# Optimization experiments

Hardware: AMD Instinct MI355X
Metric: run time of the kernel (lower is better)

The kernel has to match this reference:

```python
import jax, jax.numpy as jnp
import numpy as np

B, S, D, H = 2, 2048, 1024, 16
DH = D // H  # dim per head (dim_singl_head)
SCALE = 0.02


def layer_norm(x, g, b, eps=1e-5):
    m = jnp.mean(x, axis=-1, keepdims=True)
    v = jnp.mean((x - m) ** 2, axis=-1, keepdims=True)
    return (x - m) / jnp.sqrt(v + eps) * g + b


def setup_inputs() -> dict:
    key = jax.random.key(0)
    ks = jax.random.split(key, 12)
    return {
        "query": jax.random.normal(ks[0], (B, S, D), jnp.float32),
        "key": jax.random.normal(ks[1], (B, S, D), jnp.float32),
        "value": jax.random.normal(ks[2], (B, S, D), jnp.float32),
        "mask": jax.random.randint(ks[3], (B, S), 0, 2).astype(jnp.int32),
        "Wq": jax.random.normal(ks[4], (D, D), jnp.float32) * SCALE,
        "bq": jnp.zeros((D,), jnp.float32),
        "Wk": jax.random.normal(ks[5], (D, D), jnp.float32) * SCALE,
        "bk": jnp.zeros((D,), jnp.float32),
        "Wv": jax.random.normal(ks[6], (D, D), jnp.float32) * SCALE,
        "bv": jnp.zeros((D,), jnp.float32),
        "g_att": jnp.ones((DH,), jnp.float32),
        "b_att": jnp.zeros((DH,), jnp.float32),
        "Wres": jax.random.normal(ks[7], (D, D), jnp.float32) * SCALE,
        "bres": jnp.zeros((D,), jnp.float32),
        "g_out": jnp.ones((D,), jnp.float32),
        "b_out": jnp.zeros((D,), jnp.float32),
    }


def reference(query, key, value, mask, Wq, bq, Wk, bk, Wv, bv,
              g_att, b_att, Wres, bres, g_out, b_out):
    # split heads: torch's split(dh,-1)+cat(dim=0) == [H,B,S,dh] layout
    def heads(x):
        return x.reshape(B, S, H, DH).transpose(2, 0, 1, 3)  # [H,B,S,dh]

    q = heads(query @ Wq + bq)
    k = heads(key @ Wk + bk)
    v = heads(value @ Wv + bv)

    # additive mask: (1-mask)*-1e9, broadcast [1,B,1,Sk]
    madd = (1.0 - mask.astype(q.dtype))[None, :, None, :] * -1e9

    scores = jnp.einsum('hbqd,hbkd->hbqk', q, k) / np.float32(np.sqrt(DH))
    w = jax.nn.softmax(scores + madd, axis=-1)
    out = jnp.einsum('hbqk,hbkd->hbqd', w, v)

    out = out + q                         # residual_att
    out = layer_norm(out, g_att, b_att)   # per-head LayerNorm on dh

    # concat heads back: [H,B,S,dh] -> [B,S,H*dh]
    out = out.transpose(1, 2, 0, 3).reshape(B, S, D)

    out = out + jnp.tanh(out @ Wres + bres)  # residual_out branch
    out = layer_norm(out, g_out, b_out)      # norm_out
    return jnp.tanh(out)                     # final activation
```

## Files before the change

### kernel.cpp

```cpp
#include <hip/hip_runtime.h>
#include <cstdint>
#include <cstddef>

#define BB 2
#define SS 2048
#define DD 1024
#define HH 16
#define DHH 64
#define MROWS (BB*SS)

typedef short short8 __attribute__((ext_vector_type(8)));
typedef short short4v __attribute__((ext_vector_type(4)));
typedef float floatx4 __attribute__((ext_vector_type(4)));
typedef float floatx16 __attribute__((ext_vector_type(16)));
typedef unsigned int uint4v __attribute__((ext_vector_type(4)));

#define GAS __attribute__((address_space(1)))
#define LAS __attribute__((address_space(3)))

__device__ __forceinline__ float4 ld4(const float* p) { return *(const float4*)p; }

__device__ __forceinline__ short f2bf(float x) {
    unsigned u = __builtin_bit_cast(unsigned, x);
    unsigned r = (u + 0x7fffu + ((u >> 16) & 1u)) >> 16;
    return (short)r;
}

__device__ __forceinline__ unsigned cvtpk(float lo, float hi) {
    unsigned r;
    asm("v_cvt_pk_bf16_f32 %0, %1, %2" : "=v"(r) : "v"(lo), "v"(hi));
    return r;
}

__device__ __forceinline__ void gl_lds16(const short* g, short* l) {
    __builtin_amdgcn_global_load_lds((const GAS unsigned int*)g,
                                     (LAS unsigned int*)l, 16, 0, 0);
}

__global__ __launch_bounds__(256) void convert_kernel(
    const float* __restrict__ s0, const float* __restrict__ s1, const float* __restrict__ s2,
    short* __restrict__ d0, short* __restrict__ d1, short* __restrict__ d2)
{
    const float* s; short* d;
    if (blockIdx.z == 0)      { s = s0; d = d0; }
    else if (blockIdx.z == 1) { s = s1; d = d1; }
    else                      { s = s2; d = d2; }
    size_t idx = ((size_t)blockIdx.x * 256 + threadIdx.x) * 8;
    float4 a = ld4(s + idx);
    float4 b = ld4(s + idx + 4);
    short8 p;
    p[0] = f2bf(a.x); p[1] = f2bf(a.y); p[2] = f2bf(a.z); p[3] = f2bf(a.w);
    p[4] = f2bf(b.x); p[5] = f2bf(b.y); p[6] = f2bf(b.z); p[7] = f2bf(b.w);
    *(short8*)(d + idx) = p;
}

__global__ __launch_bounds__(256) void transpose_w_kernel(
    const float* __restrict__ W0, const float* __restrict__ W1,
    const float* __restrict__ W2, const float* __restrict__ W3,
    short* __restrict__ T0, short* __restrict__ T1,
    short* __restrict__ T2, short* __restrict__ T3)
{
    const float* W; short* T;
    if (blockIdx.z == 0)      { W = W0; T = T0; }
    else if (blockIdx.z == 1) { W = W1; T = T1; }
    else if (blockIdx.z == 2) { W = W2; T = T2; }
    else                      { W = W3; T = T3; }

    __shared__ short tile[64 * 72];
    const int t  = threadIdx.x;
    const int k0 = blockIdx.x * 64, n0 = blockIdx.y * 64;
#pragma unroll
    for (int i = 0; i < 4; i++) {
        int flat = i * 256 + t;
        int row = flat >> 4;
        int c4  = (flat & 15) * 4;
        float4 v = ld4(W + (size_t)(k0 + row) * DD + n0 + c4);
        tile[(c4 + 0) * 72 + row] = f2bf(v.x);
        tile[(c4 + 1) * 72 + row] = f2bf(v.y);
        tile[(c4 + 2) * 72 + row] = f2bf(v.z);
        tile[(c4 + 3) * 72 + row] = f2bf(v.w);
    }
    __syncthreads();
#pragma unroll
    for (int i = 0; i < 4; i++) {
        int flat = i * 256 + t;
        int nrow = flat >> 4;
        int kc   = (flat & 15) * 4;
        short4v pk = *(short4v*)&tile[nrow * 72 + kc];
        *(short4v*)(T + (size_t)(n0 + nrow) * DD + k0 + kc) = pk;
    }
}

__global__ __launch_bounds__(256) void gemm_bf16_kernel(
    const short* __restrict__ A0, const short* __restrict__ A1, const short* __restrict__ A2,
    const short* __restrict__ Bt0, const short* __restrict__ Bt1, const short* __restrict__ Bt2,
    const float* __restrict__ b0, const float* __restrict__ b1, const float* __restrict__ b2,
    float* __restrict__ Cf0, float* __restrict__ Cf1, float* __restrict__ Cf2,
    short* __restrict__ Cb0, short* __restrict__ Cb1, short* __restrict__ Cb2,
    short* __restrict__ Ct0, short* __restrict__ Ct1, short* __restrict__ Ct2,
    float cs0, float cs1, float cs2)
{
    const short* A; const short* Bt; const float* bias;
    float* Cf; short* Cb; short* Ct; float cbs;
    if (blockIdx.z == 0)      { A = A0; Bt = Bt0; bias = b0; Cf = Cf0; Cb = Cb0; Ct = Ct0; cbs = cs0; }
    else if (blockIdx.z == 1) { A = A1; Bt = Bt1; bias = b1; Cf = Cf1; Cb = Cb1; Ct = Ct1; cbs = cs1; }
    else                      { A = A2; Bt = Bt2; bias = b2; Cf = Cf2; Cb = Cb2; Ct = Ct2; cbs = cs2; }

    __shared__ __align__(16) short As[128 * 32];
    __shared__ __align__(16) short Bs[128 * 32];

    const int tid  = threadIdx.x;
    const int lane = tid & 63;
    const int wave = tid >> 6;
    const int quad = lane >> 4;
    const int l15  = lane & 15;
    const int m0 = blockIdx.y * 128;
    const int n0 = blockIdx.x * 128;
    const int wr = (wave >> 1) * 64;
    const int wc = (wave & 1) * 64;

    floatx4 acc[4][4];
#pragma unroll
    for (int mt = 0; mt < 4; mt++)
#pragma unroll
        for (int nt = 0; nt < 4; nt++) acc[mt][nt] = (floatx4)0.0f;

    for (int k0 = 0; k0 < DD; k0 += 32) {
        __syncthreads();
#pragma unroll
        for (int j = 0; j < 2; j++) {
            int chunk = j * 256 + tid;
            int row = chunk >> 2;
            int ch  = chunk & 3;
            gl_lds16(A  + (size_t)(m0 + row) * DD + k0 + ch * 8, &As[chunk * 8]);
            gl_lds16(Bt + (size_t)(n0 + row) * DD + k0 + ch * 8, &Bs[chunk * 8]);
        }
        __syncthreads();

        short8 af[4], bf[4];
#pragma unroll
        for (int mt = 0; mt < 4; mt++)
            af[mt] = *(const short8*)&As[(wr + mt * 16 + l15) * 32 + quad * 8];
#pragma unroll
        for (int nt = 0; nt < 4; nt++)
            bf[nt] = *(const short8*)&Bs[(wc + nt * 16 + l15) * 32 + quad * 8];
#pragma unroll
        for (int mt = 0; mt < 4; mt++)
#pragma unroll
            for (int nt = 0; nt < 4; nt++)
                acc[mt][nt] = __builtin_amdgcn_mfma_f32_16x16x32_bf16(af[mt], bf[nt], acc[mt][nt], 0, 0, 0);
    }

    float biasv[4];
#pragma unroll
    for (int nt = 0; nt < 4; nt++) biasv[nt] = bias[n0 + wc + nt * 16 + l15];

    if (Cf || Cb) {
#pragma unroll
        for (int mt = 0; mt < 4; mt++)
#pragma unroll
            for (int r = 0; r < 4; r++) {
                const int m = m0 + wr + mt * 16 + quad * 4 + r;
                const size_t rowb = (size_t)m * DD + n0 + wc;
#pragma unroll
                for (int nt = 0; nt < 4; nt++) {
                    float v = acc[mt][nt][r] + biasv[nt];
                    if (Cf) Cf[rowb + nt * 16 + l15] = v;
                    if (Cb) Cb[rowb + nt * 16 + l15] = f2bf(v * cbs);
                }
            }
    }
    if (Ct) {
#pragma unroll
        for (int mt = 0; mt < 4; mt++) {
            const int mbase = m0 + wr + mt * 16 + quad * 4;
            const int bb = mbase >> 11;
            const int s0 = mbase & 2047;
#pragma unroll
            for (int nt = 0; nt < 4; nt++) {
                const int c = n0 + wc + nt * 16 + l15;
                short4v pk;
#pragma unroll
                for (int r = 0; r < 4; r++) pk[r] = f2bf(acc[mt][nt][r] + biasv[nt]);
                *(short4v*)(Ct + ((size_t)(bb * 1024 + c)) * SS + s0) = pk;
            }
        }
    }
}

__global__ __launch_bounds__(256, 2) void attn_mfma_kernel(
    const short* __restrict__ Qb, const short* __restrict__ Kb, const short* __restrict__ Vt,
    const float* __restrict__ Qf, const int* __restrict__ mask,
    const float* __restrict__ g_att, const float* __restrict__ b_att,
    float* __restrict__ X, short* __restrict__ Xb)
{
    const int tid  = threadIdx.x;
    const int lane = tid & 63;
    const int wave = tid >> 6;
    const int hi   = lane >> 5;
    const int c    = lane & 31;

    const int h  = blockIdx.y;
    const int b  = blockIdx.z;
    const int q0 = blockIdx.x * 128;
    const int bS = b * SS;

    __shared__ __align__(16) short Ks[2 * 64 * 72];
    __shared__ __align__(16) short Vs[2 * 64 * 72];
    __shared__ float smadd[2 * 64];

    short8 qf[4];
#pragma unroll
    for (int ks = 0; ks < 4; ks++)
        qf[ks] = *(const short8*)(Qb +
            (size_t)(bS + q0 + wave * 32 + c) * DD + h * 64 + ks * 16 + hi * 8);

    floatx16 o[2];
    o[0] = (floatx16)0.0f;
    o[1] = (floatx16)0.0f;
    float lsum = 0.0f;

    const int srow = tid >> 3;
    const int sch  = tid & 7;

    short8 kreg[2], vreg[2];
    float mreg;
    {
#pragma unroll
        for (int i = 0; i < 2; i++) {
            int row = srow + i * 32;
            kreg[i] = *(const short8*)(Kb + (size_t)(bS + row) * DD + h * 64 + sch * 8);
            vreg[i] = *(const short8*)(Vt + (size_t)(b * 1024 + h * 64 + row) * SS + sch * 8);
        }
        mreg = (tid < 64) ? (float)mask[bS + tid] : 0.0f;
    }

    for (int kt = 0; kt < SS / 64; kt++) {
        const int bufo = (kt & 1) * (64 * 72);
#pragma unroll
        for (int i = 0; i < 2; i++) {
            int row = srow + i * 32;
            *(short8*)&Ks[bufo + row * 72 + sch * 8] = kreg[i];
            *(short8*)&Vs[bufo + row * 72 + sch * 8] = vreg[i];
        }
        if (tid < 64) smadd[(kt & 1) * 64 + tid] = (1.0f - mreg) * -1e9f;

        if (kt < SS / 64 - 1) {
            const int k0n = (kt + 1) * 64;
#pragma unroll
            for (int i = 0; i < 2; i++) {
                int row = srow + i * 32;
                kreg[i] = *(const short8*)(Kb + (size_t)(bS + k0n + row) * DD + h * 64 + sch * 8);
                vreg[i] = *(const short8*)(Vt + (size_t)(b * 1024 + h * 64 + row) * SS + k0n + sch * 8);
            }
            mreg = (tid < 64) ? (float)mask[bS + k0n + tid] : 0.0f;
        }

        __builtin_amdgcn_s_waitcnt(0xC07F);
        __builtin_amdgcn_s_barrier();

#pragma unroll
        for (int g = 0; g < 2; g++) {
            floatx16 acc = (floatx16)0.0f;
#pragma unroll
            for (int ks = 0; ks < 4; ks++) {
                short8 kf = *(const short8*)&Ks[bufo + (g * 32 + c) * 72 + ks * 16 + hi * 8];
                acc = __builtin_amdgcn_mfma_f32_32x32x16_bf16(kf, qf[ks], acc, 0, 0, 0);
            }
            float p[16];
#pragma unroll
            for (int a = 0; a < 4; a++) {
                float4 mr = *(const float4*)&smadd[(kt & 1) * 64 + g * 32 + a * 8 + hi * 4];
                p[4 * a + 0] = __builtin_exp2f(acc[4 * a + 0] + mr.x);
                p[4 * a + 1] = __builtin_exp2f(acc[4 * a + 1] + mr.y);
                p[4 * a + 2] = __builtin_exp2f(acc[4 * a + 2] + mr.z);
                p[4 * a + 3] = __builtin_exp2f(acc[4 * a + 3] + mr.w);
            }
            lsum += ((p[0] + p[1]) + (p[2] + p[3])) + ((p[4] + p[5]) + (p[6] + p[7]))
                  + ((p[8] + p[9]) + (p[10] + p[11])) + ((p[12] + p[13]) + (p[14] + p[15]));

#pragma unroll
            for (int t = 0; t < 2; t++) {
                unsigned w0 = cvtpk(p[8 * t + 0], p[8 * t + 1]);
                unsigned w1 = cvtpk(p[8 * t + 2], p[8 * t + 3]);
                unsigned w2 = cvtpk(p[8 * t + 4], p[8 * t + 5]);
                unsigned w3 = cvtpk(p[8 * t + 6], p[8 * t + 7]);
                asm volatile("v_permlane32_swap_b32 %0, %1" : "+v"(w0), "+v"(w2));
                asm volatile("v_permlane32_swap_b32 %0, %1" : "+v"(w1), "+v"(w3));
                uint4v u = {w0, w1, w2, w3};
                short8 pa = __builtin_bit_cast(short8, u);
#pragma unroll
                for (int dg = 0; dg < 2; dg++) {
                    short8 vb = *(const short8*)&Vs[bufo + (dg * 32 + c) * 72
                                                    + (g * 2 + t) * 16 + hi * 8];
                    o[dg] = __builtin_amdgcn_mfma_f32_32x32x16_bf16(pa, vb, o[dg], 0, 0, 0);
                }
            }
        }
    }

    lsum += __shfl_xor(lsum, 32);
    const float rl = 1.0f / lsum;

    const float g0v = g_att[c], g1v = g_att[32 + c];
    const float b0v = b_att[c], b1v = b_att[32 + c];

#pragma unroll
    for (int r = 0; r < 16; r++) {
        const int rloc = (r & 3) + 8 * (r >> 2) + 4 * hi;
        const float rlr = __shfl(rl, rloc);
        const int row = q0 + wave * 32 + rloc;
        const size_t base = (size_t)(bS + row) * DD + h * 64;
        float x0 = o[0][r] * rlr + Qf[base + c];
        float x1 = o[1][r] * rlr + Qf[base + 32 + c];
        float s = x0 + x1;
#pragma unroll
        for (int off = 1; off < 32; off <<= 1) s += __shfl_xor(s, off);
        const float mu = s * (1.0f / 64.0f);
        float d0 = x0 - mu, d1 = x1 - mu;
        float v = d0 * d0 + d1 * d1;
#pragma unroll
        for (int off = 1; off < 32; off <<= 1) v += __shfl_xor(v, off);
        const float rstd = rsqrtf(v * (1.0f / 64.0f) + 1e-5f);
        float y0 = d0 * rstd * g0v + b0v;
        float y1 = d1 * rstd * g1v + b1v;
        X[base + c]      = y0;
        X[base + 32 + c] = y1;
        Xb[base + c]      = f2bf(y0);
        Xb[base + 32 + c] = f2bf(y1);
    }
}

__global__ __launch_bounds__(256) void lnout_kernel(
    const float* __restrict__ X, const float* __restrict__ Y,
    const float* __restrict__ g, const float* __restrict__ bcoef,
    float* __restrict__ out)
{
    const int r = blockIdx.x;
    const int t = threadIdx.x;
    const size_t base = (size_t)r * DD + (t << 2);
    float4 x = ld4(X + base);
    float4 y = ld4(Y + base);
    float4 z;
    z.x = x.x + tanhf(y.x);
    z.y = x.y + tanhf(y.y);
    z.z = x.z + tanhf(y.z);
    z.w = x.w + tanhf(y.w);

    __shared__ float red[4];
    __shared__ float stats[2];
    const int w = t >> 6;

    float sv = z.x + z.y + z.z + z.w;
#pragma unroll
    for (int off = 32; off > 0; off >>= 1) sv += __shfl_down(sv, off);
    if ((t & 63) == 0) red[w] = sv;
    __syncthreads();
    if (t == 0) stats[0] = (red[0] + red[1] + red[2] + red[3]) * (1.0f / 1024.0f);
    __syncthreads();
    const float mu = stats[0];

    float4 d;
    d.x = z.x - mu; d.y = z.y - mu; d.z = z.z - mu; d.w = z.w - mu;
    float s2 = d.x * d.x + d.y * d.y + d.z * d.z + d.w * d.w;
#pragma unroll
    for (int off = 32; off > 0; off >>= 1) s2 += __shfl_down(s2, off);
    if ((t & 63) == 0) red[w] = s2;
    __syncthreads();
    if (t == 0) stats[1] = rsqrtf((red[0] + red[1] + red[2] + red[3]) * (1.0f / 1024.0f) + 1e-5f);
    __syncthreads();
    const float rstd = stats[1];

    float4 gv = ld4(g + (t << 2));
    float4 bv = ld4(bcoef + (t << 2));
    float4 o;
    o.x = tanhf(d.x * rstd * gv.x + bv.x);
    o.y = tanhf(d.y * rstd * gv.y + bv.y);
    o.z = tanhf(d.z * rstd * gv.z + bv.z);
    o.w = tanhf(d.w * rstd * gv.w + bv.w);
    *(float4*)(out + base) = o;
}

extern "C" void kernel_launch(void* const* d_in, const int* in_sizes, int n_in,
                              void* d_out, int out_size, void* d_ws, size_t ws_size,
                              hipStream_t stream)
{
    const float* query = (const float*)d_in[0];
    const float* key   = (const float*)d_in[1];
    const float* value = (const float*)d_in[2];
    const int*   mask  = (const int*)  d_in[3];
    const float* Wq    = (const float*)d_in[4];
    const float* bq    = (const float*)d_in[5];
    const float* Wk    = (const float*)d_in[6];
    const float* bk    = (const float*)d_in[7];
    const float* Wv    = (const float*)d_in[8];
    const float* bv    = (const float*)d_in[9];
    const float* g_att = (const float*)d_in[10];
    const float* b_att = (const float*)d_in[11];
    const float* Wres  = (const float*)d_in[12];
    const float* bres  = (const float*)d_in[13];
    const float* g_out = (const float*)d_in[14];
    const float* b_out = (const float*)d_in[15];

    const size_t MAT = (size_t)MROWS * DD;
    float* fws = (float*)d_ws;
    float* Qw = fws;
    float* Xw = fws + MAT;
    short* Qb = (short*)(fws + 2 * MAT);
    short* Kb = Qb + MAT;
    short* Vt = Kb + MAT;
    short* qbf = Vt + MAT;
    short* kbf = qbf + MAT;
    short* vbf = kbf + MAT;
    short* Wtq = vbf + MAT;
    short* Wtk = Wtq + DD * DD;
    short* Wtv = Wtk + DD * DD;
    short* Wtr = Wtv + DD * DD;
    short* Xb = qbf;
    float* Yw = (float*)kbf;

    convert_kernel<<<dim3(MAT / 2048, 1, 3), 256, 0, stream>>>(
        query, key, value, qbf, kbf, vbf);

    transpose_w_kernel<<<dim3(16, 16, 4), 256, 0, stream>>>(
        Wq, Wk, Wv, Wres, Wtq, Wtk, Wtv, Wtr);

    gemm_bf16_kernel<<<dim3(8, 32, 3), 256, 0, stream>>>(
        qbf, kbf, vbf, Wtq, Wtk, Wtv, bq, bk, bv,
        Qw, nullptr, nullptr,
        Qb, Kb, nullptr,
        nullptr, nullptr, Vt,
        0.180336884f, 1.0f, 1.0f);

    attn_mfma_kernel<<<dim3(SS / 128, HH, BB), 256, 0, stream>>>(
        Qb, Kb, Vt, Qw, mask, g_att, b_att, Xw, Xb);

    gemm_bf16_kernel<<<dim3(8, 32, 1), 256, 0, stream>>>(
        Xb, Xb, Xb, Wtr, Wtr, Wtr, bres, bres, bres,
        Yw, Yw, Yw, nullptr, nullptr, nullptr, nullptr, nullptr, nullptr,
        1.0f, 1.0f, 1.0f);

    lnout_kernel<<<MROWS, 256, 0, stream>>>(Xw, Yw, g_out, b_out, (float*)d_out);
}
```

Before: 290.3 us.

## Repack K/V into MFMA fragment layout and stream directly from global into registers

Adds a repack kernel that rearranges K and transposed V into per-head, per-tile MFMA fragment order and precomputes the additive mask as floats. The attention kernel then drops its LDS staging, double buffering and barriers, loading fragments with coalesced per-lane global reads into registers, software-pipelined one tile ahead, with MFMA sections raised via s_setprio. This trades LDS traffic and block synchronisation for an extra kernel launch, more register pressure, and redundant global/L2 reads since each block now fetches its own K/V fragments.

```diff
diff --git a/kernel.cpp b/kernel.cpp
--- a/kernel.cpp
+++ b/kernel.cpp
@@ -188,9 +188,91 @@
     }
 }
 
+__global__ __launch_bounds__(256) void repack_kernel(
+    const short* __restrict__ Kb, const short* __restrict__ Vt,
+    const int* __restrict__ mask,
+    short* __restrict__ Kf, short* __restrict__ Vf, float* __restrict__ maddf)
+{
+    const int t = threadIdx.x;
+    if (blockIdx.z == 0) {
+        const int b = blockIdx.x >> 6, kg = blockIdx.x & 63;
+#pragma unroll
+        for (int i = 0; i < 16; i++) {
+            const int h = i, ks = t >> 6, lane = t & 63;
+            const int c = lane & 31, hi = lane >> 5;
+            short8 v = *(const short8*)(Kb + (size_t)(b * 2048 + kg * 32 + c) * 1024
+                                        + h * 64 + ks * 16 + hi * 8);
+            *(short8*)(Kf + ((size_t)((b * 16 + h) * 64 + kg)) * 2048 + ks * 512 + lane * 8) = v;
+        }
+    } else if (blockIdx.x < 64) {
+        const int b = blockIdx.x >> 5, kt = blockIdx.x & 31;
+#pragma unroll
+        for (int i = 0; i < 32; i++) {
+            const int flat = i * 256 + t;
+            const int h = flat >> 9, rest = flat & 511;
+            const int tp = rest >> 7, dg = (rest >> 6) & 1, lane = rest & 63;
+            const int c = lane & 31, hi = lane >> 5;
+            short8 v = *(const short8*)(Vt + (size_t)(b * 1024 + h * 64 + dg * 32 + c) * 2048
+                                        + kt * 64 + tp * 16 + hi * 8);
+            *(short8*)(Vf + ((size_t)((b * 16 + h) * 32 + kt)) * 4096
+                       + (tp * 2 + dg) * 512 + lane * 8) = v;
+        }
+    } else if (blockIdx.x < 66) {
+        const int b = blockIdx.x - 64;
+#pragma unroll
+        for (int j = 0; j < 8; j++) {
+            const int idx = t * 8 + j;
+            maddf[b * 2048 + idx] = (1.0f - (float)mask[b * 2048 + idx]) * -1e9f;
+        }
+    }
+}
+
+__device__ __forceinline__ void attn_tile(
+    const short8 (&kf)[2][4], const short8 (&vf)[8], const short8 (&qf)[4],
+    const float* mdb, int kt, floatx16 (&o)[2], float& lsum)
+{
+#pragma unroll
+    for (int g = 0; g < 2; g++) {
+        floatx16 acc = (floatx16)0.0f;
+        __builtin_amdgcn_s_setprio(1);
+#pragma unroll
+        for (int ks = 0; ks < 4; ks++)
+            acc = __builtin_amdgcn_mfma_f32_32x32x16_bf16(kf[g][ks], qf[ks], acc, 0, 0, 0);
+        __builtin_amdgcn_s_setprio(0);
+        float p[16];
+#pragma unroll
+        for (int a = 0; a < 4; a++) {
+            float4 mr = *(const float4*)(mdb + kt * 64 + g * 32 + a * 8);
+            p[4 * a + 0] = __builtin_exp2f(acc[4 * a + 0] + mr.x);
+            p[4 * a + 1] = __builtin_exp2f(acc[4 * a + 1] + mr.y);
+            p[4 * a + 2] = __builtin_exp2f(acc[4 * a + 2] + mr.z);
+            p[4 * a + 3] = __builtin_exp2f(acc[4 * a + 3] + mr.w);
+        }
+        lsum += ((p[0] + p[1]) + (p[2] + p[3])) + ((p[4] + p[5]) + (p[6] + p[7]))
+              + ((p[8] + p[9]) + (p[10] + p[11])) + ((p[12] + p[13]) + (p[14] + p[15]));
+#pragma unroll
+        for (int t2 = 0; t2 < 2; t2++) {
+            unsigned w0 = cvtpk(p[8 * t2 + 0], p[8 * t2 + 1]);
+            unsigned w1 = cvtpk(p[8 * t2 + 2], p[8 * t2 + 3]);
+            unsigned w2 = cvtpk(p[8 * t2 + 4], p[8 * t2 + 5]);
+            unsigned w3 = cvtpk(p[8 * t2 + 6], p[8 * t2 + 7]);
+            asm volatile("v_permlane32_swap_b32 %0, %1" : "+v"(w0), "+v"(w2));
+            asm volatile("v_permlane32_swap_b32 %0, %1" : "+v"(w1), "+v"(w3));
+            uint4v u = {w0, w1, w2, w3};
+            short8 pa = __builtin_bit_cast(short8, u);
+            __builtin_amdgcn_s_setprio(1);
+#pragma unroll
+            for (int dg = 0; dg < 2; dg++)
+                o[dg] = __builtin_amdgcn_mfma_f32_32x32x16_bf16(
+                    pa, vf[(g * 2 + t2) * 2 + dg], o[dg], 0, 0, 0);
+            __builtin_amdgcn_s_setprio(0);
+        }
+    }
+}
+
 __global__ __launch_bounds__(256, 2) void attn_mfma_kernel(
-    const short* __restrict__ Qb, const short* __restrict__ Kb, const short* __restrict__ Vt,
-    const float* __restrict__ Qf, const int* __restrict__ mask,
+    const short* __restrict__ Qb, const short* __restrict__ Kf, const short* __restrict__ Vf,
+    const float* __restrict__ Qf, const float* __restrict__ maddf,
     const float* __restrict__ g_att, const float* __restrict__ b_att,
     float* __restrict__ X, short* __restrict__ Xb)
 {
@@ -205,9 +287,9 @@
     const int q0 = blockIdx.x * 128;
     const int bS = b * SS;
 
-    __shared__ __align__(16) short Ks[2 * 64 * 72];
-    __shared__ __align__(16) short Vs[2 * 64 * 72];
-    __shared__ float smadd[2 * 64];
+    const short* kfb = Kf + ((size_t)(b * 16 + h) * 64) * 2048 + lane * 8;
+    const short* vfb = Vf + ((size_t)(b * 16 + h) * 32) * 4096 + lane * 8;
+    const float* mdb = maddf + b * 2048 + hi * 4;
 
     short8 qf[4];
 #pragma unroll
@@ -220,83 +302,34 @@
     o[1] = (floatx16)0.0f;
     float lsum = 0.0f;
 
-    const int srow = tid >> 3;
-    const int sch  = tid & 7;
-
-    short8 kreg[2], vreg[2];
-    float mreg;
-    {
-#pragma unroll
-        for (int i = 0; i < 2; i++) {
-            int row = srow + i * 32;
-            kreg[i] = *(const short8*)(Kb + (size_t)(bS + row) * DD + h * 64 + sch * 8);
-            vreg[i] = *(const short8*)(Vt + (size_t)(b * 1024 + h * 64 + row) * SS + sch * 8);
-        }
-        mreg = (tid < 64) ? (float)mask[bS + tid] : 0.0f;
-    }
-
-    for (int kt = 0; kt < SS / 64; kt++) {
-        const int bufo = (kt & 1) * (64 * 72);
-#pragma unroll
-        for (int i = 0; i < 2; i++) {
-            int row = srow + i * 32;
-            *(short8*)&Ks[bufo + row * 72 + sch * 8] = kreg[i];
-            *(short8*)&Vs[bufo + row * 72 + sch * 8] = vreg[i];
-        }
-        if (tid < 64) smadd[(kt & 1) * 64 + tid] = (1.0f - mreg) * -1e9f;
-
-        if (kt < SS / 64 - 1) {
-            const int k0n = (kt + 1) * 64;
-#pragma unroll
-            for (int i = 0; i < 2; i++) {
-                int row = srow + i * 32;
-                kreg[i] = *(const short8*)(Kb + (size_t)(bS + k0n + row) * DD + h * 64 + sch * 8);
-                vreg[i] = *(const short8*)(Vt + (size_t)(b * 1024 + h * 64 + row) * SS + k0n + sch * 8);
-            }
-            mreg = (tid < 64) ? (float)mask[bS + k0n + tid] : 0.0f;
-        }
-
-        __builtin_amdgcn_s_waitcnt(0xC07F);
-        __builtin_amdgcn_s_barrier();
-
-#pragma unroll
-        for (int g = 0; g < 2; g++) {
-            floatx16 acc = (floatx16)0.0f;
-#pragma unroll
-            for (int ks = 0; ks < 4; ks++) {
-                short8 kf = *(const short8*)&Ks[bufo + (g * 32 + c) * 72 + ks * 16 + hi * 8];
-                acc = __builtin_amdgcn_mfma_f32_32x32x16_bf16(kf, qf[ks], acc, 0, 0, 0);
-            }
-            float p[16];
-#pragma unroll
-            for (int a = 0; a < 4; a++) {
-                float4 mr = *(const float4*)&smadd[(kt & 1) * 64 + g * 32 + a * 8 + hi * 4];
-                p[4 * a + 0] = __builtin_exp2f(acc[4 * a + 0] + mr.x);
-                p[4 * a + 1] = __builtin_exp2f(acc[4 * a + 1] + mr.y);
-                p[4 * a + 2] = __builtin_exp2f(acc[4 * a + 2] + mr.z);
-                p[4 * a + 3] = __builtin_exp2f(acc[4 * a + 3] + mr.w);
-            }
-            lsum += ((p[0] + p[1]) + (p[2] + p[3])) + ((p[4] + p[5]) + (p[6] + p[7]))
-                  + ((p[8] + p[9]) + (p[10] + p[11])) + ((p[12] + p[13]) + (p[14] + p[15]));
-
-#pragma unroll
-            for (int t = 0; t < 2; t++) {
-                unsigned w0 = cvtpk(p[8 * t + 0], p[8 * t + 1]);
-                unsigned w1 = cvtpk(p[8 * t + 2], p[8 * t + 3]);
-                unsigned w2 = cvtpk(p[8 * t + 4], p[8 * t + 5]);
-                unsigned w3 = cvtpk(p[8 * t + 6], p[8 * t + 7]);
-                asm volatile("v_permlane32_swap_b32 %0, %1" : "+v"(w0), "+v"(w2));
-                asm volatile("v_permlane32_swap_b32 %0, %1" : "+v"(w1), "+v"(w3));
-                uint4v u = {w0, w1, w2, w3};
-                short8 pa = __builtin_bit_cast(short8, u);
-#pragma unroll
-                for (int dg = 0; dg < 2; dg++) {
-                    short8 vb = *(const short8*)&Vs[bufo + (dg * 32 + c) * 72
-                                                    + (g * 2 + t) * 16 + hi * 8];
-                    o[dg] = __builtin_amdgcn_mfma_f32_32x32x16_bf16(pa, vb, o[dg], 0, 0, 0);
-                }
-            }
-        }
+    short8 kfA[2][4], kfB[2][4], vf[8];
+#pragma unroll
+    for (int g = 0; g < 2; g++)
+#pragma unroll
+        for (int ks = 0; ks < 4; ks++)
+            kfA[g][ks] = *(const short8*)(kfb + (size_t)(0 * 2 + g) * 2048 + ks * 512);
+
+    for (int kt = 0; kt < 32; kt += 2) {
+#pragma unroll
+        for (int j = 0; j < 8; j++)
+            vf[j] = *(const short8*)(vfb + (size_t)kt * 4096 + j * 512);
+#pragma unroll
+        for (int g = 0; g < 2; g++)
+#pragma unroll
+            for (int ks = 0; ks < 4; ks++)
+                kfB[g][ks] = *(const short8*)(kfb + (size_t)((kt + 1) * 2 + g) * 2048 + ks * 512);
+        attn_tile(kfA, vf, qf, mdb, kt, o, lsum);
+
+#pragma unroll
+        for (int j = 0; j < 8; j++)
+            vf[j] = *(const short8*)(vfb + (size_t)(kt + 1) * 4096 + j * 512);
+        const int ktn = (kt + 2 < 32) ? (kt + 2) : 31;
+#pragma unroll
+        for (int g = 0; g < 2; g++)
+#pragma unroll
+            for (int ks = 0; ks < 4; ks++)
+                kfA[g][ks] = *(const short8*)(kfb + (size_t)(ktn * 2 + g) * 2048 + ks * 512);
+        attn_tile(kfB, vf, qf, mdb, kt + 1, o, lsum);
     }
 
     lsum += __shfl_xor(lsum, 32);
@@ -416,7 +449,10 @@
     short* Wtk = Wtq + DD * DD;
     short* Wtv = Wtk + DD * DD;
     short* Wtr = Wtv + DD * DD;
+    float* maddf = (float*)(Wtr + DD * DD);
     short* Xb = qbf;
+    short* Kf = vbf;
+    short* Vf = kbf;
     float* Yw = (float*)kbf;
 
     convert_kernel<<<dim3(MAT / 2048, 1, 3), 256, 0, stream>>>(
@@ -432,8 +468,11 @@
         nullptr, nullptr, Vt,
         0.180336884f, 1.0f, 1.0f);
 
+    repack_kernel<<<dim3(128, 1, 2), 256, 0, stream>>>(
+        Kb, Vt, mask, Kf, Vf, maddf);
+
     attn_mfma_kernel<<<dim3(SS / 128, HH, BB), 256, 0, stream>>>(
-        Qb, Kb, Vt, Qw, mask, g_att, b_att, Xw, Xb);
+        Qb, Kf, Vf, Qw, maddf, g_att, b_att, Xw, Xb);
 
     gemm_bf16_kernel<<<dim3(8, 32, 1), 256, 0, stream>>>(
         Xb, Xb, Xb, Wtr, Wtr, Wtr, bres, bres, bres,
```

Result: slower. 305.9 us (+5.4%).
